# Optimization experiments

Hardware: AMD Instinct MI355X
Metric: run time of the kernel (lower is better)

Reference implementation:

```python
import jax, jax.numpy as jnp
import numpy as np

EMBED_DIM = 256
NUM_HEADS = 4
HEAD_DIM = EMBED_DIM // NUM_HEADS
B, N0, N1 = 4, 2048, 2048


def setup_inputs() -> dict:
    key = jax.random.key(0)
    ks = jax.random.split(key, 16)
    d = EMBED_DIM
    s = 0.02
    return {
        "x0": jax.random.normal(ks[0], (B, N0, d), jnp.float32),
        "x1": jax.random.normal(ks[1], (B, N1, d), jnp.float32),
        "Wqk": jax.random.normal(ks[2], (d, d), jnp.float32) * s,
        "bqk": jnp.zeros((d,), jnp.float32),
        "Wv": jax.random.normal(ks[3], (d, d), jnp.float32) * s,
        "bv": jnp.zeros((d,), jnp.float32),
        "Wout": jax.random.normal(ks[4], (d, d), jnp.float32) * s,
        "bout": jnp.zeros((d,), jnp.float32),
        "W0": jax.random.normal(ks[5], (2 * d, 2 * d), jnp.float32) * s,
        "b0": jnp.zeros((2 * d,), jnp.float32),
        "ln_scale": jnp.ones((2 * d,), jnp.float32),
        "ln_bias": jnp.zeros((2 * d,), jnp.float32),
        "W3": jax.random.normal(ks[6], (2 * d, d), jnp.float32) * s,
        "b3": jnp.zeros((d,), jnp.float32),
    }


def _heads(t, b, n):
    # [b, n, d] -> [b, h, n, hd]
    return t.reshape(b, n, NUM_HEADS, HEAD_DIM).transpose(0, 2, 1, 3)


def _layernorm(y, scale, bias, eps=1e-5):
    mu = jnp.mean(y, axis=-1, keepdims=True)
    var = jnp.mean(jnp.square(y - mu), axis=-1, keepdims=True)
    return (y - mu) * jax.lax.rsqrt(var + eps) * scale + bias


def reference(x0, x1, Wqk, bqk, Wv, bv, Wout, bout, W0, b0, ln_scale, ln_bias, W3, b3):
    b, n0, d = x0.shape
    _, n1, _ = x1.shape
    scale = 1.0 / jnp.sqrt(jnp.float32(HEAD_DIM))

    qk0 = _heads(x0 @ Wqk + bqk, b, n0)
    qk1 = _heads(x1 @ Wqk + bqk, b, n1)
    v0 = _heads(x0 @ Wv + bv, b, n0)
    v1 = _heads(x1 @ Wv + bv, b, n1)

    # shared logits: [b, h, n0, n1]
    logits01 = jnp.einsum('bhid,bhjd->bhij', qk0, qk1) * scale
    attn01 = jax.nn.softmax(logits01, axis=-1)
    m0 = jnp.einsum('bhij,bhjd->bhid', attn01, v1)
    attn10 = jax.nn.softmax(logits01.transpose(0, 1, 3, 2), axis=-1)
    m1 = jnp.einsum('bhji,bhjd->bhid', attn10.transpose(0, 1, 3, 2), v0)

    m0 = m0.transpose(0, 2, 1, 3).reshape(b, n0, d) @ Wout + bout
    m1 = m1.transpose(0, 2, 1, 3).reshape(b, n1, d) @ Wout + bout

    def ffn(x, m):
        y = jnp.concatenate([x, m], axis=-1) @ W0 + b0
        y = _layernorm(y, ln_scale, ln_bias)
        y = jax.nn.gelu(y, approximate=False)
        return x + y @ W3 + b3

    return ffn(x0, m0), ffn(x1, m1)
```

## Files before the change

### kernel.cpp

```cpp
#include <hip/hip_runtime.h>
#include <math.h>

#define BATCH 4
#define SEQ 2048
#define DMODEL 256
#define NH 4
#define HD 64
#define MROWS 8192
#define QKSCALE 0.4246608905f

typedef short bf16x8 __attribute__((ext_vector_type(8)));
typedef float f32x4 __attribute__((ext_vector_type(4)));
typedef unsigned short us;

#if __has_builtin(__builtin_amdgcn_exp2f)
#define EXP2(x) __builtin_amdgcn_exp2f(x)
#else
#define EXP2(x) exp2f(x)
#endif

__device__ __forceinline__ us f2bf(float x) {
  union { float f; unsigned int u; } v;
  v.f = x;
  unsigned int r = (v.u + 0x7FFF + ((v.u >> 16) & 1)) >> 16;
  return (us)r;
}
__device__ __forceinline__ float bf2f(us u) {
  union { unsigned int u; float f; } v;
  v.u = ((unsigned int)u) << 16;
  return v.f;
}
__device__ __forceinline__ unsigned int fbits(float x) {
  union { float f; unsigned int u; } v;
  v.f = x;
  return v.u;
}
__device__ __forceinline__ unsigned int pk2bf(float lo, float hi) {
  return __builtin_amdgcn_perm(fbits(hi), fbits(lo), 0x07060302u);
}
__device__ __forceinline__ void dma16(const void* g, void* l) {
  auto gp = (const __attribute__((address_space(1))) unsigned int*)(unsigned long long)(uintptr_t)g;
  auto lp = (__attribute__((address_space(3))) unsigned int*)(unsigned int)(uintptr_t)l;
  __builtin_amdgcn_global_load_lds(gp, lp, 16, 0, 0);
}

__global__ __launch_bounds__(256) void prep_k(
    const float* __restrict__ x0, const float* __restrict__ x1,
    const float* __restrict__ Wqk, const float* __restrict__ Wv,
    const float* __restrict__ W0, const float* __restrict__ W3,
    const float* __restrict__ Wout,
    const float* __restrict__ bqk, const float* __restrict__ bv,
    const float* __restrict__ b0, const float* __restrict__ bout,
    us* __restrict__ x0b, us* __restrict__ x1b,
    us* __restrict__ Wqvt, us* __restrict__ W1t, us* __restrict__ W3t,
    float* __restrict__ bias_qv, float* __restrict__ bias1) {
  const int bid = blockIdx.x, t = threadIdx.x;
  if (bid < 4096) {
    const int n4 = (MROWS * DMODEL) / 4;
    int i = bid * 256 + t;
    const float* src = (i < n4) ? x0 : x1;
    us* dst = (i < n4) ? x0b : x1b;
    int j = (i < n4) ? i : i - n4;
    float4 v = *(const float4*)&src[j * 4];
    ushort4 o = {f2bf(v.x), f2bf(v.y), f2bf(v.z), f2bf(v.w)};
    *(ushort4*)&dst[j * 4] = o;
  } else if (bid < 5634) {
    int gid = (bid - 4096) * 256 + t;
    if (gid < 65536) {
      int k = gid >> 8, j = gid & 255;
      Wqvt[j * 256 + k] = f2bf(Wqk[gid]);
    } else if (gid < 131072) {
      int i = gid - 65536;
      int k = i >> 8, j = i & 255;
      Wqvt[(256 + j) * 256 + k] = f2bf(Wv[i]);
    } else if (gid < 262144) {
      int i = gid - 131072;
      int k = i >> 9, j = i & 511;
      W1t[j * 512 + k] = f2bf(W0[i]);
    } else if (gid < 393216) {
      int i = gid - 262144;
      int k = i >> 8, j = i & 255;
      W3t[j * 512 + k] = f2bf(W3[i]);
    } else if (gid < 393728) {
      int j = gid - 393216;
      bias_qv[j] = (j < 256) ? bqk[j] : bv[j - 256];
    }
  } else {
    int i = bid - 5634;
    if (i < 256) {
      float a0 = 0.f, a1 = 0.f;
      for (int k0 = 0; k0 < 256; k0 += 8) {
        float wk[8], r0[8], r1[8];
#pragma unroll
        for (int u = 0; u < 8; ++u) {
          wk[u] = Wout[i * 256 + k0 + u];
          const float* row = &W0[(size_t)(256 + k0 + u) * 512];
          r0[u] = row[t];
          r1[u] = row[t + 256];
        }
#pragma unroll
        for (int u = 0; u < 8; ++u) { a0 += wk[u] * r0[u]; a1 += wk[u] * r1[u]; }
      }
      W1t[t * 512 + 256 + i] = f2bf(a0);
      W1t[(t + 256) * 512 + 256 + i] = f2bf(a1);
    } else {
      float a0 = b0[t], a1 = b0[t + 256];
      for (int k = 0; k < 256; ++k) {
        float bk = bout[k];
        const float* row = &W0[(size_t)(256 + k) * 512];
        a0 += bk * row[t];
        a1 += bk * row[t + 256];
      }
      bias1[t] = a0;
      bias1[t + 256] = a1;
    }
  }
}

template <int MODE>
__global__ __launch_bounds__(256) void gemm6(
    const us* __restrict__ A0, const us* __restrict__ A1,
    const us* __restrict__ Am0, const us* __restrict__ Am1,
    const us* __restrict__ Wt, const float* __restrict__ bias,
    const float* __restrict__ r0_, const float* __restrict__ r1_,
    void* __restrict__ C0_, void* __restrict__ C1_,
    void* __restrict__ V0_, void* __restrict__ V1_, int K) {
  constexpr int CT = (MODE == 2) ? 64 : 128;
  constexpr int BG = (CT / 16) * 2;
  constexpr int BUFS = 8192 + BG * 512;
  __shared__ us lds[2 * BUFS];

  const int t = threadIdx.x, w = t >> 6, lane = t & 63;
  const int qd = lane >> 4, l15 = lane & 15;

  const int flat = blockIdx.x + 64 * (blockIdx.y + 4 * blockIdx.z);
  const int xcd = flat & 7, slot = flat >> 3;
  const int xz = (xcd << 4) + (slot >> 2);
  const int bx = xz & 63, z = xz >> 6, coltile = slot & 3;
  const int row0 = bx * 128, col0 = coltile * CT;

  const us* Ax = z ? A1 : A0;
  const us* Am = z ? Am1 : Am0;
  const int qr = (MODE == 2) ? w : (w >> 1);
  const int qc = (MODE == 2) ? 0 : (w & 1);
  constexpr int MI = (MODE == 2) ? 2 : 4;

  f32x4 acc[MI][4];
#pragma unroll
  for (int i = 0; i < MI; ++i)
#pragma unroll
    for (int j = 0; j < 4; ++j) acc[i][j] = (f32x4){0.f, 0.f, 0.f, 0.f};

  const int NK = K >> 6;
#pragma unroll
  for (int pp = 0; pp < (16 + BG) / 4; ++pp) {
    int g = pp * 4 + w;
    const us* src;
    if (g < 16) {
      int tm = g >> 1, s = g & 1;
      int kk = s * 32 + qd * 8;
      src = &Ax[(size_t)(row0 + tm * 16 + l15) * ((MODE == 1) ? 256 : K) + kk];
    } else {
      int gb = g - 16, tn = gb >> 1, s = gb & 1;
      src = &Wt[(size_t)(col0 + tn * 16 + l15) * K + s * 32 + qd * 8];
    }
    dma16(src, &lds[g * 512]);
  }
  __syncthreads();

  int bsel = 0;
  for (int it = 0; it < NK; ++it) {
    if (it + 1 < NK) {
      int k0 = (it + 1) << 6;
#pragma unroll
      for (int pp = 0; pp < (16 + BG) / 4; ++pp) {
        int g = pp * 4 + w;
        const us* src;
        if (g < 16) {
          int tm = g >> 1, s = g & 1;
          const us* Ap = Ax;
          int kk = k0 + s * 32 + qd * 8, lda = K;
          if (MODE == 1) {
            Ap = (k0 < 256) ? Ax : Am;
            kk &= 255;
            lda = 256;
          }
          src = &Ap[(size_t)(row0 + tm * 16 + l15) * lda + kk];
        } else {
          int gb = g - 16, tn = gb >> 1, s = gb & 1;
          src = &Wt[(size_t)(col0 + tn * 16 + l15) * K + k0 + s * 32 + qd * 8];
        }
        dma16(src, &lds[(bsel ^ 1) * BUFS + g * 512]);
      }
    }
    const us* L = &lds[bsel * BUFS];
#pragma unroll
    for (int s = 0; s < 2; ++s) {
      bf16x8 af[MI], bfr[4];
#pragma unroll
      for (int i = 0; i < MI; ++i)
        af[i] = *(const bf16x8*)&L[(((qr * MI + i) * 2 + s) * 64 + lane) * 8];
#pragma unroll
      for (int j = 0; j < 4; ++j)
        bfr[j] = *(const bf16x8*)&L[8192 + (((qc * 4 + j) * 2 + s) * 64 + lane) * 8];
#pragma unroll
      for (int i = 0; i < MI; ++i)
#pragma unroll
        for (int j = 0; j < 4; ++j)
          acc[i][j] = __builtin_amdgcn_mfma_f32_16x16x32_bf16(af[i], bfr[j], acc[i][j], 0, 0, 0);
    }
    __syncthreads();
    bsel ^= 1;
  }

  if (MODE == 0 && coltile >= 2) {
    int base = qc * 8320;
#pragma unroll
    for (int j = 0; j < 4; ++j) {
      int col = col0 + qc * 64 + j * 16 + l15;
      float bb = bias[col];
#pragma unroll
      for (int i = 0; i < 4; ++i)
#pragma unroll
        for (int r = 0; r < 4; ++r)
          lds[base + (j * 16 + l15) * 130 + (qr * 64 + i * 16 + qd * 4 + r)] =
              f2bf(acc[i][j][r] + bb);
    }
    __syncthreads();
    us* Vt = (us*)(z ? V1_ : V0_);
    int b_ = row0 >> 11, seq0 = row0 & 2047;
    for (int c = t; c < 2048; c += 256) {
      int hh = c >> 10, cc = c & 1023;
      int dloc = cc >> 4, scc = cc & 15;
      int h = (coltile - 2) * 2 + hh;
      uint4 d = *(const uint4*)&lds[hh * 8320 + dloc * 130 + scc * 8];
      *(uint4*)&Vt[((size_t)(b_ * NH + h) * HD + dloc) * SEQ + seq0 + scc * 8] = d;
    }
    return;
  }

  if (MODE == 0 || MODE == 1) {
#pragma unroll
    for (int j = 0; j < 4; ++j) {
      int cl = qc * 64 + j * 16 + l15;
      float bb = bias[col0 + cl];
#pragma unroll
      for (int i = 0; i < 4; ++i)
#pragma unroll
        for (int r = 0; r < 4; ++r) {
          float v = acc[i][j][r] + bb;
          if (MODE == 0) v *= QKSCALE;
          lds[(qr * 64 + i * 16 + qd * 4 + r) * 132 + cl] = f2bf(v);
        }
    }
    __syncthreads();
    us* C = (us*)(z ? C1_ : C0_);
    const int ldc = (MODE == 0) ? 256 : 512;
    for (int c = t; c < 2048; c += 256) {
      int rl = c >> 4, c8 = (c & 15) * 8;
      uint4 d = *(const uint4*)&lds[rl * 132 + c8];
      *(uint4*)&C[(size_t)(row0 + rl) * ldc + col0 + c8] = d;
    }
    return;
  }

#pragma unroll
  for (int j = 0; j < 4; ++j) {
    int col = col0 + j * 16 + l15;
    float bb = bias[col];
#pragma unroll
    for (int i = 0; i < MI; ++i)
#pragma unroll
      for (int r = 0; r < 4; ++r) {
        size_t grow = row0 + qr * (MI * 16) + i * 16 + qd * 4 + r;
        const float* R = z ? r1_ : r0_;
        ((float*)(z ? C1_ : C0_))[grow * 256 + col] =
            R[grow * 256 + col] + acc[i][j][r] + bb;
      }
  }
}

__global__ __launch_bounds__(256) void flash_v7(
    const us* __restrict__ qk0, const us* __restrict__ qk1,
    const us* __restrict__ vt0, const us* __restrict__ vt1,
    float* __restrict__ Opart, float* __restrict__ lpart) {
  __shared__ us lds[16384];
  const int t = threadIdx.x, w = t >> 6, lane = t & 63;
  const int qd = lane >> 4, l15 = lane & 15;

  const int flat = blockIdx.x + 32 * (blockIdx.y + 4 * blockIdx.z);
  const int xcd = flat & 7, slot = flat >> 3;
  const int combo = (xcd << 2) + (slot >> 5);
  const int qs = slot & 31;
  const int qt = qs & 15, half = qs >> 4;
  const int dir = combo >> 4, bh = combo & 15, b = bh >> 2, h = bh & 3;

  const us* Qb = dir ? qk1 : qk0;
  const us* Kb = dir ? qk0 : qk1;
  const us* Vt = dir ? vt0 : vt1;
  float* Op = Opart + (size_t)(dir * 2 + half) * (MROWS * DMODEL);
  float* lp = lpart + ((size_t)(dir * 2 + half) * NH + h) * MROWS;
  const size_t qrow0 = (size_t)b * SEQ + (size_t)qt * 128;
  const int hoff = h * HD;
  const us* vtb = Vt + (size_t)(b * NH + h) * HD * SEQ;
  const int kt0 = half * 16;

  const us* sp[4];
  int sstr[4];
#pragma unroll
  for (int pp = 0; pp < 4; ++pp) {
    int g = pp * 4 + w;
    if (g < 8) {
      int tk = g >> 1, s = g & 1;
      int kvl = (tk >> 1) * 32 + (l15 >> 2) * 8 + (tk & 1) * 4 + (l15 & 3);
      sp[pp] = &Kb[(size_t)(b * SEQ + kt0 * 64 + kvl) * DMODEL + hoff + s * 32 + qd * 8];
      sstr[pp] = 64 * DMODEL;
    } else {
      int td = (g - 8) >> 1, s = g & 1;
      sp[pp] = &vtb[(size_t)(td * 16 + l15) * SEQ + kt0 * 64 + s * 32 + qd * 8];
      sstr[pp] = 64;
    }
  }

  bf16x8 qf[2][2];
#pragma unroll
  for (int qh = 0; qh < 2; ++qh)
#pragma unroll
    for (int s = 0; s < 2; ++s)
      qf[qh][s] = *(const bf16x8*)&Qb[(qrow0 + w * 32 + qh * 16 + l15) * DMODEL + hoff + s * 32 + qd * 8];

  f32x4 Oacc[2][4];
#pragma unroll
  for (int qh = 0; qh < 2; ++qh)
#pragma unroll
    for (int td = 0; td < 4; ++td) Oacc[qh][td] = (f32x4){0.f, 0.f, 0.f, 0.f};
  float l_lane[2] = {0.f, 0.f};

#pragma unroll
  for (int pp = 0; pp < 4; ++pp) {
    dma16(sp[pp], &lds[(pp * 4 + w) * 512]);
    sp[pp] += sstr[pp];
  }
  __syncthreads();

  int bsel = 0;
  for (int it = 0; it < 16; ++it) {
    if (it < 15) {
#pragma unroll
      for (int pp = 0; pp < 4; ++pp) {
        dma16(sp[pp], &lds[(bsel ^ 1) * 8192 + (pp * 4 + w) * 512]);
        sp[pp] += sstr[pp];
      }
    }
    const us* L = &lds[bsel * 8192];

    bf16x8 kf[4][2], vf[4][2];
#pragma unroll
    for (int tk = 0; tk < 4; ++tk)
#pragma unroll
      for (int s = 0; s < 2; ++s) {
        kf[tk][s] = *(const bf16x8*)&L[((tk * 2 + s) * 64 + lane) * 8];
        vf[tk][s] = *(const bf16x8*)&L[((8 + tk * 2 + s) * 64 + lane) * 8];
      }

#pragma unroll
    for (int qh = 0; qh < 2; ++qh) {
      f32x4 S[4];
#pragma unroll
      for (int tk = 0; tk < 4; ++tk) {
        f32x4 a = {0.f, 0.f, 0.f, 0.f};
        a = __builtin_amdgcn_mfma_f32_16x16x32_bf16(kf[tk][0], qf[qh][0], a, 0, 0, 0);
        a = __builtin_amdgcn_mfma_f32_16x16x32_bf16(kf[tk][1], qf[qh][1], a, 0, 0, 0);
        S[tk] = a;
      }
      float p[4][4];
      float rs = 0.f;
#pragma unroll
      for (int tk = 0; tk < 4; ++tk)
#pragma unroll
        for (int r = 0; r < 4; ++r) {
          float pv = EXP2(S[tk][r]);
          p[tk][r] = pv;
          rs += pv;
        }
      l_lane[qh] += rs;
      union { bf16x8 v; unsigned int u[4]; } pk0, pk1;
      pk0.u[0] = pk2bf(p[0][0], p[0][1]);
      pk0.u[1] = pk2bf(p[0][2], p[0][3]);
      pk0.u[2] = pk2bf(p[1][0], p[1][1]);
      pk0.u[3] = pk2bf(p[1][2], p[1][3]);
      pk1.u[0] = pk2bf(p[2][0], p[2][1]);
      pk1.u[1] = pk2bf(p[2][2], p[2][3]);
      pk1.u[2] = pk2bf(p[3][0], p[3][1]);
      pk1.u[3] = pk2bf(p[3][2], p[3][3]);
#pragma unroll
      for (int td = 0; td < 4; ++td) {
        Oacc[qh][td] = __builtin_amdgcn_mfma_f32_16x16x32_bf16(pk0.v, vf[td][0], Oacc[qh][td], 0, 0, 0);
        Oacc[qh][td] = __builtin_amdgcn_mfma_f32_16x16x32_bf16(pk1.v, vf[td][1], Oacc[qh][td], 0, 0, 0);
      }
    }
    __syncthreads();
    bsel ^= 1;
  }

#pragma unroll
  for (int qh = 0; qh < 2; ++qh) {
    float l = l_lane[qh];
    l += __shfl_xor(l, 16);
    l += __shfl_xor(l, 32);
    if (qd == 0) lp[qrow0 + w * 32 + qh * 16 + l15] = l;
#pragma unroll
    for (int r = 0; r < 4; ++r) {
      size_t row = qrow0 + w * 32 + qh * 16 + qd * 4 + r;
#pragma unroll
      for (int td = 0; td < 4; ++td)
        Op[row * DMODEL + hoff + td * 16 + l15] = Oacc[qh][td][r];
    }
  }
}

__global__ __launch_bounds__(256) void combine_k(
    const float* __restrict__ Opart, const float* __restrict__ lpart,
    us* __restrict__ m0b, us* __restrict__ m1b) {
  int gid = blockIdx.x * 256 + threadIdx.x;
  int dir = gid >= (MROWS * DMODEL / 4);
  int idx = gid - dir * (MROWS * DMODEL / 4);
  int row = idx >> 6;
  int c4 = (idx & 63) << 2;
  int h = c4 >> 6;
  const float* Oa = Opart + (size_t)(dir * 2 + 0) * (MROWS * DMODEL);
  const float* Ob = Opart + (size_t)(dir * 2 + 1) * (MROWS * DMODEL);
  float la = lpart[((size_t)(dir * 2 + 0) * NH + h) * MROWS + row];
  float lb = lpart[((size_t)(dir * 2 + 1) * NH + h) * MROWS + row];
  float inv = 1.0f / (la + lb);
  float4 a = *(const float4*)&Oa[(size_t)row * DMODEL + c4];
  float4 bv = *(const float4*)&Ob[(size_t)row * DMODEL + c4];
  us* m = dir ? m1b : m0b;
  ushort4 o = {f2bf((a.x + bv.x) * inv), f2bf((a.y + bv.y) * inv),
               f2bf((a.z + bv.z) * inv), f2bf((a.w + bv.w) * inv)};
  *(ushort4*)&m[(size_t)row * DMODEL + c4] = o;
}

__global__ __launch_bounds__(256) void ln_gelu3(
    us* __restrict__ Y0, us* __restrict__ Y1,
    const float* __restrict__ sc, const float* __restrict__ bi) {
  int w = threadIdx.x >> 6, lane = threadIdx.x & 63;
  int ridx = blockIdx.x * 4 + w;
  us* Y = (ridx >= MROWS) ? Y1 : Y0;
  int row = ridx & (MROWS - 1);
  us* p = Y + (size_t)row * 512 + lane * 8;
  uint4 u = *(const uint4*)p;
  unsigned int uu[4] = {u.x, u.y, u.z, u.w};
  float v[8];
#pragma unroll
  for (int i = 0; i < 4; ++i) {
    v[2 * i] = bf2f((us)(uu[i] & 0xFFFF));
    v[2 * i + 1] = bf2f((us)(uu[i] >> 16));
  }
  float s1 = 0.f, s2 = 0.f;
#pragma unroll
  for (int i = 0; i < 8; ++i) { s1 += v[i]; s2 += v[i] * v[i]; }
#pragma unroll
  for (int m = 1; m < 64; m <<= 1) {
    s1 += __shfl_xor(s1, m);
    s2 += __shfl_xor(s2, m);
  }
  float mu = s1 * (1.0f / 512.0f);
  float var = s2 * (1.0f / 512.0f) - mu * mu;
  float rstd = rsqrtf(var + 1e-5f);
  int c0 = lane * 8;
  float4 scA = *(const float4*)&sc[c0], scB = *(const float4*)&sc[c0 + 4];
  float4 biA = *(const float4*)&bi[c0], biB = *(const float4*)&bi[c0 + 4];
  float scv[8] = {scA.x, scA.y, scA.z, scA.w, scB.x, scB.y, scB.z, scB.w};
  float biv[8] = {biA.x, biA.y, biA.z, biA.w, biB.x, biB.y, biB.z, biB.w};
  unsigned int ou[4];
#pragma unroll
  for (int i = 0; i < 4; ++i) {
    float y0 = (v[2 * i] - mu) * rstd * scv[2 * i] + biv[2 * i];
    float y1 = (v[2 * i + 1] - mu) * rstd * scv[2 * i + 1] + biv[2 * i + 1];
    y0 = 0.5f * y0 * (1.0f + erff(y0 * 0.70710678118654752f));
    y1 = 0.5f * y1 * (1.0f + erff(y1 * 0.70710678118654752f));
    ou[i] = (unsigned int)f2bf(y0) | ((unsigned int)f2bf(y1) << 16);
  }
  uint4 o = {ou[0], ou[1], ou[2], ou[3]};
  *(uint4*)p = o;
}

extern "C" void kernel_launch(void* const* d_in, const int* in_sizes, int n_in,
                              void* d_out, int out_size, void* d_ws,
                              size_t ws_size, hipStream_t stream) {
  const float* x0   = (const float*)d_in[0];
  const float* x1   = (const float*)d_in[1];
  const float* Wqk  = (const float*)d_in[2];
  const float* bqk  = (const float*)d_in[3];
  const float* Wv   = (const float*)d_in[4];
  const float* bv   = (const float*)d_in[5];
  const float* Wout = (const float*)d_in[6];
  const float* bout = (const float*)d_in[7];
  const float* W0   = (const float*)d_in[8];
  const float* b0   = (const float*)d_in[9];
  const float* lns  = (const float*)d_in[10];
  const float* lnb  = (const float*)d_in[11];
  const float* W3   = (const float*)d_in[12];
  const float* b3   = (const float*)d_in[13];

  char* ws = (char*)d_ws;
  const size_t MB = 1024 * 1024;
  us* x0b  = (us*)(ws + 0 * MB);
  us* x1b  = (us*)(ws + 4 * MB);
  us* Wqvt = (us*)(ws + 8 * MB);
  us* W1t  = (us*)(ws + 8 * MB + 262144);
  us* W3t  = (us*)(ws + 8 * MB + 786432);
  float* bias_qv = (float*)(ws + 9 * MB);
  float* bias1   = (float*)(ws + 9 * MB + 4096);
  us* qk0b = (us*)(ws + 10 * MB);
  us* qk1b = (us*)(ws + 14 * MB);
  us* vt0  = (us*)(ws + 18 * MB);
  us* vt1  = (us*)(ws + 22 * MB);
  us* m0b  = (us*)(ws + 26 * MB);
  us* m1b  = (us*)(ws + 30 * MB);
  us* y0b  = (us*)(ws + 10 * MB);
  us* y1b  = (us*)(ws + 18 * MB);
  float* Opart = (float*)(ws + 34 * MB);
  float* lpart = (float*)(ws + 66 * MB);
  float* out0 = (float*)d_out;
  float* out1 = out0 + (size_t)MROWS * DMODEL;

  dim3 blk(256);

  prep_k<<<dim3(5891), blk, 0, stream>>>(x0, x1, Wqk, Wv, W0, W3, Wout,
                                         bqk, bv, b0, bout,
                                         x0b, x1b, Wqvt, W1t, W3t,
                                         bias_qv, bias1);

  gemm6<0><<<dim3(64, 4, 2), blk, 0, stream>>>(
      x0b, x1b, nullptr, nullptr, Wqvt, bias_qv, nullptr, nullptr,
      qk0b, qk1b, vt0, vt1, 256);

  flash_v7<<<dim3(32, 4, 8), blk, 0, stream>>>(qk0b, qk1b, vt0, vt1, Opart, lpart);
  combine_k<<<dim3(4096), blk, 0, stream>>>(Opart, lpart, m0b, m1b);

  gemm6<1><<<dim3(64, 4, 2), blk, 0, stream>>>(
      x0b, x1b, m0b, m1b, W1t, bias1, nullptr, nullptr,
      y0b, y1b, nullptr, nullptr, 512);

  ln_gelu3<<<dim3(4096), blk, 0, stream>>>(y0b, y1b, lns, lnb);

  gemm6<2><<<dim3(64, 4, 2), blk, 0, stream>>>(
      y0b, y1b, nullptr, nullptr, W3t, b3, x0, x1,
      out0, out1, nullptr, nullptr, 512);
}
```

Baseline: 234.8 us.

## Fuse split-KV combine into flash kernel and LayerNorm-GELU into FFN GEMMs

```diff
diff --git a/kernel.cpp b/kernel.cpp
--- a/kernel.cpp
+++ b/kernel.cpp
@@ -53,7 +53,8 @@
     const float* __restrict__ b0, const float* __restrict__ bout,
     us* __restrict__ x0b, us* __restrict__ x1b,
     us* __restrict__ Wqvt, us* __restrict__ W1t, us* __restrict__ W3t,
-    float* __restrict__ bias_qv, float* __restrict__ bias1) {
+    float* __restrict__ bias_qv, float* __restrict__ bias1,
+    float* __restrict__ zbase) {
   const int bid = blockIdx.x, t = threadIdx.x;
   if (bid < 4096) {
     const int n4 = (MROWS * DMODEL) / 4;
@@ -85,7 +86,7 @@
       int j = gid - 393216;
       bias_qv[j] = (j < 256) ? bqk[j] : bv[j - 256];
     }
-  } else {
+  } else if (bid < 5891) {
     int i = bid - 5634;
     if (i < 256) {
       float a0 = 0.f, a1 = 0.f;
@@ -114,6 +115,12 @@
       bias1[t] = a0;
       bias1[t + 256] = a1;
     }
+  } else {
+    int i = (bid - 5891) * 256 + t;
+    if (i * 4 < 33792) {
+      float4 zz = {0.f, 0.f, 0.f, 0.f};
+      *(float4*)&zbase[i * 4] = zz;
+    }
   }
 }
 
@@ -122,12 +129,10 @@
     const us* __restrict__ A0, const us* __restrict__ A1,
     const us* __restrict__ Am0, const us* __restrict__ Am1,
     const us* __restrict__ Wt, const float* __restrict__ bias,
-    const float* __restrict__ r0_, const float* __restrict__ r1_,
     void* __restrict__ C0_, void* __restrict__ C1_,
-    void* __restrict__ V0_, void* __restrict__ V1_, int K) {
-  constexpr int CT = (MODE == 2) ? 64 : 128;
-  constexpr int BG = (CT / 16) * 2;
-  constexpr int BUFS = 8192 + BG * 512;
+    void* __restrict__ V0_, void* __restrict__ V1_, int K,
+    float* __restrict__ lnsum, float* __restrict__ lnsq) {
+  constexpr int BUFS = 16384;
   __shared__ us lds[2 * BUFS];
 
   const int t = threadIdx.x, w = t >> 6, lane = t & 63;
@@ -137,29 +142,26 @@
   const int xcd = flat & 7, slot = flat >> 3;
   const int xz = (xcd << 4) + (slot >> 2);
   const int bx = xz & 63, z = xz >> 6, coltile = slot & 3;
-  const int row0 = bx * 128, col0 = coltile * CT;
+  const int row0 = bx * 128, col0 = coltile * 128;
 
   const us* Ax = z ? A1 : A0;
   const us* Am = z ? Am1 : Am0;
-  const int qr = (MODE == 2) ? w : (w >> 1);
-  const int qc = (MODE == 2) ? 0 : (w & 1);
-  constexpr int MI = (MODE == 2) ? 2 : 4;
-
-  f32x4 acc[MI][4];
-#pragma unroll
-  for (int i = 0; i < MI; ++i)
+  const int qr = w >> 1, qc = w & 1;
+
+  f32x4 acc[4][4];
+#pragma unroll
+  for (int i = 0; i < 4; ++i)
 #pragma unroll
     for (int j = 0; j < 4; ++j) acc[i][j] = (f32x4){0.f, 0.f, 0.f, 0.f};
 
   const int NK = K >> 6;
 #pragma unroll
-  for (int pp = 0; pp < (16 + BG) / 4; ++pp) {
+  for (int pp = 0; pp < 8; ++pp) {
     int g = pp * 4 + w;
     const us* src;
     if (g < 16) {
       int tm = g >> 1, s = g & 1;
-      int kk = s * 32 + qd * 8;
-      src = &Ax[(size_t)(row0 + tm * 16 + l15) * ((MODE == 1) ? 256 : K) + kk];
+      src = &Ax[(size_t)(row0 + tm * 16 + l15) * ((MODE == 1) ? 256 : K) + s * 32 + qd * 8];
     } else {
       int gb = g - 16, tn = gb >> 1, s = gb & 1;
       src = &Wt[(size_t)(col0 + tn * 16 + l15) * K + s * 32 + qd * 8];
@@ -173,7 +175,7 @@
     if (it + 1 < NK) {
       int k0 = (it + 1) << 6;
 #pragma unroll
-      for (int pp = 0; pp < (16 + BG) / 4; ++pp) {
+      for (int pp = 0; pp < 8; ++pp) {
         int g = pp * 4 + w;
         const us* src;
         if (g < 16) {
@@ -196,15 +198,14 @@
     const us* L = &lds[bsel * BUFS];
 #pragma unroll
     for (int s = 0; s < 2; ++s) {
-      bf16x8 af[MI], bfr[4];
-#pragma unroll
-      for (int i = 0; i < MI; ++i)
-        af[i] = *(const bf16x8*)&L[(((qr * MI + i) * 2 + s) * 64 + lane) * 8];
-#pragma unroll
-      for (int j = 0; j < 4; ++j)
-        bfr[j] = *(const bf16x8*)&L[8192 + (((qc * 4 + j) * 2 + s) * 64 + lane) * 8];
-#pragma unroll
-      for (int i = 0; i < MI; ++i)
+      bf16x8 af[4], bfr[4];
+#pragma unroll
+      for (int i = 0; i < 4; ++i) {
+        af[i] = *(const bf16x8*)&L[(((qr * 4 + i) * 2 + s) * 64 + lane) * 8];
+        bfr[i] = *(const bf16x8*)&L[8192 + (((qc * 4 + i) * 2 + s) * 64 + lane) * 8];
+      }
+#pragma unroll
+      for (int i = 0; i < 4; ++i)
 #pragma unroll
         for (int j = 0; j < 4; ++j)
           acc[i][j] = __builtin_amdgcn_mfma_f32_16x16x32_bf16(af[i], bfr[j], acc[i][j], 0, 0, 0);
@@ -239,52 +240,59 @@
     return;
   }
 
-  if (MODE == 0 || MODE == 1) {
-#pragma unroll
-    for (int j = 0; j < 4; ++j) {
-      int cl = qc * 64 + j * 16 + l15;
-      float bb = bias[col0 + cl];
-#pragma unroll
-      for (int i = 0; i < 4; ++i)
-#pragma unroll
-        for (int r = 0; r < 4; ++r) {
-          float v = acc[i][j][r] + bb;
-          if (MODE == 0) v *= QKSCALE;
-          lds[(qr * 64 + i * 16 + qd * 4 + r) * 132 + cl] = f2bf(v);
-        }
-    }
-    __syncthreads();
-    us* C = (us*)(z ? C1_ : C0_);
-    const int ldc = (MODE == 0) ? 256 : 512;
-    for (int c = t; c < 2048; c += 256) {
-      int rl = c >> 4, c8 = (c & 15) * 8;
-      uint4 d = *(const uint4*)&lds[rl * 132 + c8];
-      *(uint4*)&C[(size_t)(row0 + rl) * ldc + col0 + c8] = d;
-    }
-    return;
-  }
-
 #pragma unroll
   for (int j = 0; j < 4; ++j) {
-    int col = col0 + j * 16 + l15;
-    float bb = bias[col];
-#pragma unroll
-    for (int i = 0; i < MI; ++i)
+    int cl = qc * 64 + j * 16 + l15;
+    float bb = bias[col0 + cl];
+#pragma unroll
+    for (int i = 0; i < 4; ++i)
 #pragma unroll
       for (int r = 0; r < 4; ++r) {
-        size_t grow = row0 + qr * (MI * 16) + i * 16 + qd * 4 + r;
-        const float* R = z ? r1_ : r0_;
-        ((float*)(z ? C1_ : C0_))[grow * 256 + col] =
-            R[grow * 256 + col] + acc[i][j][r] + bb;
-      }
-  }
-}
-
-__global__ __launch_bounds__(256) void flash_v7(
+        float v = acc[i][j][r] + bb;
+        if (MODE == 0) v *= QKSCALE;
+        lds[(qr * 64 + i * 16 + qd * 4 + r) * 132 + cl] = f2bf(v);
+      }
+  }
+  __syncthreads();
+  us* C = (us*)(z ? C1_ : C0_);
+  const int ldc = (MODE == 0) ? 256 : 512;
+  for (int c = t; c < 2048; c += 256) {
+    int rl = c >> 4, c8 = (c & 15) * 8;
+    uint4 d = *(const uint4*)&lds[rl * 132 + c8];
+    *(uint4*)&C[(size_t)(row0 + rl) * ldc + col0 + c8] = d;
+  }
+
+  if (MODE == 1) {
+    int rl = t >> 1, hf = t & 1;
+    float s1 = 0.f, s2 = 0.f;
+#pragma unroll
+    for (int c = 0; c < 64; c += 8) {
+      uint4 d = *(const uint4*)&lds[rl * 132 + hf * 64 + c];
+      unsigned int uu[4] = {d.x, d.y, d.z, d.w};
+#pragma unroll
+      for (int i = 0; i < 4; ++i) {
+        float a = bf2f((us)(uu[i] & 0xFFFF));
+        float b = bf2f((us)(uu[i] >> 16));
+        s1 += a + b;
+        s2 += a * a + b * b;
+      }
+    }
+    s1 += __shfl_xor(s1, 1);
+    s2 += __shfl_xor(s2, 1);
+    if (hf == 0) {
+      atomicAdd(&lnsum[z * MROWS + row0 + rl], s1);
+      atomicAdd(&lnsq[z * MROWS + row0 + rl], s2);
+    }
+  }
+}
+
+__global__ __launch_bounds__(256) void flash_v8(
     const us* __restrict__ qk0, const us* __restrict__ qk1,
     const us* __restrict__ vt0, const us* __restrict__ vt1,
-    float* __restrict__ Opart, float* __restrict__ lpart) {
+    float* __restrict__ Opart, float* __restrict__ lpart,
+    us* __restrict__ m0b, us* __restrict__ m1b, int* __restrict__ tickets) {
   __shared__ us lds[16384];
+  __shared__ int sOld;
   const int t = threadIdx.x, w = t >> 6, lane = t & 63;
   const int qd = lane >> 4, l15 = lane & 15;
 
@@ -403,11 +411,13 @@
     bsel ^= 1;
   }
 
+  float lred[2];
 #pragma unroll
   for (int qh = 0; qh < 2; ++qh) {
     float l = l_lane[qh];
     l += __shfl_xor(l, 16);
     l += __shfl_xor(l, 32);
+    lred[qh] = l;
     if (qd == 0) lp[qrow0 + w * 32 + qh * 16 + l15] = l;
 #pragma unroll
     for (int r = 0; r < 4; ++r) {
@@ -417,73 +427,137 @@
         Op[row * DMODEL + hoff + td * 16 + l15] = Oacc[qh][td][r];
     }
   }
-}
-
-__global__ __launch_bounds__(256) void combine_k(
-    const float* __restrict__ Opart, const float* __restrict__ lpart,
-    us* __restrict__ m0b, us* __restrict__ m1b) {
-  int gid = blockIdx.x * 256 + threadIdx.x;
-  int dir = gid >= (MROWS * DMODEL / 4);
-  int idx = gid - dir * (MROWS * DMODEL / 4);
-  int row = idx >> 6;
-  int c4 = (idx & 63) << 2;
-  int h = c4 >> 6;
-  const float* Oa = Opart + (size_t)(dir * 2 + 0) * (MROWS * DMODEL);
-  const float* Ob = Opart + (size_t)(dir * 2 + 1) * (MROWS * DMODEL);
-  float la = lpart[((size_t)(dir * 2 + 0) * NH + h) * MROWS + row];
-  float lb = lpart[((size_t)(dir * 2 + 1) * NH + h) * MROWS + row];
-  float inv = 1.0f / (la + lb);
-  float4 a = *(const float4*)&Oa[(size_t)row * DMODEL + c4];
-  float4 bv = *(const float4*)&Ob[(size_t)row * DMODEL + c4];
-  us* m = dir ? m1b : m0b;
-  ushort4 o = {f2bf((a.x + bv.x) * inv), f2bf((a.y + bv.y) * inv),
-               f2bf((a.z + bv.z) * inv), f2bf((a.w + bv.w) * inv)};
-  *(ushort4*)&m[(size_t)row * DMODEL + c4] = o;
-}
-
-__global__ __launch_bounds__(256) void ln_gelu3(
-    us* __restrict__ Y0, us* __restrict__ Y1,
+
+  __threadfence();
+  __syncthreads();
+  if (t == 0) sOld = atomicAdd(&tickets[((dir * BATCH + b) * NH + h) * 16 + qt], 1);
+  __syncthreads();
+  if (sOld == 1) {
+    __threadfence();
+    us* m = dir ? m1b : m0b;
+    const float* Opp = Opart + (size_t)(dir * 2 + (half ^ 1)) * (MROWS * DMODEL);
+    const float* lpp = lpart + ((size_t)(dir * 2 + (half ^ 1)) * NH + h) * MROWS;
+#pragma unroll
+    for (int qh = 0; qh < 2; ++qh) {
+      float inv = 1.0f / (lred[qh] + lpp[qrow0 + w * 32 + qh * 16 + l15]);
+#pragma unroll
+      for (int r = 0; r < 4; ++r) {
+        float lq = __shfl(inv, qd * 20 + r, 64);
+        size_t row = qrow0 + w * 32 + qh * 16 + qd * 4 + r;
+#pragma unroll
+        for (int td = 0; td < 4; ++td) {
+          float o = Oacc[qh][td][r] + Opp[row * DMODEL + hoff + td * 16 + l15];
+          m[row * DMODEL + hoff + td * 16 + l15] = f2bf(o * lq);
+        }
+      }
+    }
+  }
+}
+
+__global__ __launch_bounds__(256) void ffn2_k(
+    const us* __restrict__ y0b, const us* __restrict__ y1b,
+    const us* __restrict__ W3t, const float* __restrict__ b3,
+    const float* __restrict__ x0, const float* __restrict__ x1,
+    float* __restrict__ out0, float* __restrict__ out1,
+    const float* __restrict__ lnsum, const float* __restrict__ lnsq,
     const float* __restrict__ sc, const float* __restrict__ bi) {
-  int w = threadIdx.x >> 6, lane = threadIdx.x & 63;
-  int ridx = blockIdx.x * 4 + w;
-  us* Y = (ridx >= MROWS) ? Y1 : Y0;
-  int row = ridx & (MROWS - 1);
-  us* p = Y + (size_t)row * 512 + lane * 8;
-  uint4 u = *(const uint4*)p;
-  unsigned int uu[4] = {u.x, u.y, u.z, u.w};
-  float v[8];
-#pragma unroll
-  for (int i = 0; i < 4; ++i) {
-    v[2 * i] = bf2f((us)(uu[i] & 0xFFFF));
-    v[2 * i + 1] = bf2f((us)(uu[i] >> 16));
-  }
-  float s1 = 0.f, s2 = 0.f;
-#pragma unroll
-  for (int i = 0; i < 8; ++i) { s1 += v[i]; s2 += v[i] * v[i]; }
-#pragma unroll
-  for (int m = 1; m < 64; m <<= 1) {
-    s1 += __shfl_xor(s1, m);
-    s2 += __shfl_xor(s2, m);
-  }
-  float mu = s1 * (1.0f / 512.0f);
-  float var = s2 * (1.0f / 512.0f) - mu * mu;
-  float rstd = rsqrtf(var + 1e-5f);
-  int c0 = lane * 8;
-  float4 scA = *(const float4*)&sc[c0], scB = *(const float4*)&sc[c0 + 4];
-  float4 biA = *(const float4*)&bi[c0], biB = *(const float4*)&bi[c0 + 4];
-  float scv[8] = {scA.x, scA.y, scA.z, scA.w, scB.x, scB.y, scB.z, scB.w};
-  float biv[8] = {biA.x, biA.y, biA.z, biA.w, biB.x, biB.y, biB.z, biB.w};
-  unsigned int ou[4];
-#pragma unroll
-  for (int i = 0; i < 4; ++i) {
-    float y0 = (v[2 * i] - mu) * rstd * scv[2 * i] + biv[2 * i];
-    float y1 = (v[2 * i + 1] - mu) * rstd * scv[2 * i + 1] + biv[2 * i + 1];
-    y0 = 0.5f * y0 * (1.0f + erff(y0 * 0.70710678118654752f));
-    y1 = 0.5f * y1 * (1.0f + erff(y1 * 0.70710678118654752f));
-    ou[i] = (unsigned int)f2bf(y0) | ((unsigned int)f2bf(y1) << 16);
-  }
-  uint4 o = {ou[0], ou[1], ou[2], ou[3]};
-  *(uint4*)p = o;
+  constexpr int BUFS = 12288;
+  __shared__ us lds[2 * BUFS];
+  const int t = threadIdx.x, w = t >> 6, lane = t & 63;
+  const int qd = lane >> 4, l15 = lane & 15;
+
+  const int flat = blockIdx.x + 128 * (blockIdx.y + 2 * blockIdx.z);
+  const int xcd = flat & 7, slot = flat >> 3;
+  const int xz = xcd * 32 + (slot >> 1);
+  const int bx = xz & 127, z = xz >> 7, ct = slot & 1;
+  const int row0 = bx * 64, col0 = ct * 128;
+
+  const us* Y = z ? y1b : y0b;
+  const float* lsum = lnsum + z * MROWS;
+  const float* lsq = lnsq + z * MROWS;
+  const int qr = w >> 1, qc = w & 1;
+
+  f32x4 acc[2][4];
+#pragma unroll
+  for (int i = 0; i < 2; ++i)
+#pragma unroll
+    for (int j = 0; j < 4; ++j) acc[i][j] = (f32x4){0.f, 0.f, 0.f, 0.f};
+
+  auto stage = [&](int k0, us* buf) {
+#pragma unroll
+    for (int pp = 0; pp < 4; ++pp) {
+      int gb = pp * 4 + w;
+      int tn = gb >> 1, s = gb & 1;
+      dma16(&W3t[(size_t)(col0 + tn * 16 + l15) * 512 + k0 + s * 32 + qd * 8],
+            &buf[4096 + gb * 512]);
+    }
+#pragma unroll
+    for (int pp = 0; pp < 2; ++pp) {
+      int g = pp * 4 + w;
+      int tm = g >> 1, s = g & 1;
+      int row = row0 + tm * 16 + l15;
+      int kk = k0 + s * 32 + qd * 8;
+      uint4 d = *(const uint4*)&Y[(size_t)row * 512 + kk];
+      float mu = lsum[row] * (1.0f / 512.0f);
+      float vr = lsq[row] * (1.0f / 512.0f) - mu * mu;
+      float rstd = rsqrtf(vr + 1e-5f);
+      unsigned int uu[4] = {d.x, d.y, d.z, d.w};
+      unsigned int ou[4];
+#pragma unroll
+      for (int i = 0; i < 4; ++i) {
+        int k_ = kk + 2 * i;
+        float a = bf2f((us)(uu[i] & 0xFFFF));
+        float bq = bf2f((us)(uu[i] >> 16));
+        float g0 = (a - mu) * rstd * sc[k_] + bi[k_];
+        float g1 = (bq - mu) * rstd * sc[k_ + 1] + bi[k_ + 1];
+        g0 = 0.5f * g0 * (1.0f + erff(g0 * 0.70710678118654752f));
+        g1 = 0.5f * g1 * (1.0f + erff(g1 * 0.70710678118654752f));
+        ou[i] = pk2bf(g0, g1);
+      }
+      uint4 o = {ou[0], ou[1], ou[2], ou[3]};
+      *(uint4*)&buf[g * 512 + lane * 8] = o;
+    }
+  };
+
+  stage(0, lds);
+  __syncthreads();
+  int bsel = 0;
+  for (int it = 0; it < 8; ++it) {
+    if (it < 7) stage((it + 1) * 64, &lds[(bsel ^ 1) * BUFS]);
+    const us* L = &lds[bsel * BUFS];
+#pragma unroll
+    for (int s = 0; s < 2; ++s) {
+      bf16x8 af[2], bfr[4];
+#pragma unroll
+      for (int i = 0; i < 2; ++i)
+        af[i] = *(const bf16x8*)&L[(((qr * 2 + i) * 2 + s) * 64 + lane) * 8];
+#pragma unroll
+      for (int j = 0; j < 4; ++j)
+        bfr[j] = *(const bf16x8*)&L[4096 + (((qc * 4 + j) * 2 + s) * 64 + lane) * 8];
+#pragma unroll
+      for (int i = 0; i < 2; ++i)
+#pragma unroll
+        for (int j = 0; j < 4; ++j)
+          acc[i][j] = __builtin_amdgcn_mfma_f32_16x16x32_bf16(af[i], bfr[j], acc[i][j], 0, 0, 0);
+    }
+    __syncthreads();
+    bsel ^= 1;
+  }
+
+  const float* X = z ? x1 : x0;
+  float* O = z ? out1 : out0;
+#pragma unroll
+  for (int j = 0; j < 4; ++j) {
+    int col = col0 + qc * 64 + j * 16 + l15;
+    float bb = b3[col];
+#pragma unroll
+    for (int i = 0; i < 2; ++i)
+#pragma unroll
+      for (int r = 0; r < 4; ++r) {
+        size_t grow = row0 + qr * 32 + i * 16 + qd * 4 + r;
+        O[grow * 256 + col] = X[grow * 256 + col] + acc[i][j][r] + bb;
+      }
+  }
 }
 
 extern "C" void kernel_launch(void* const* d_in, const int* in_sizes, int n_in,
@@ -523,30 +597,31 @@
   us* y1b  = (us*)(ws + 18 * MB);
   float* Opart = (float*)(ws + 34 * MB);
   float* lpart = (float*)(ws + 66 * MB);
+  int* tickets = (int*)(ws + 66 * MB + 524288);
+  float* lnsum = (float*)(ws + 66 * MB + 528384);
+  float* lnsq  = lnsum + 2 * MROWS;
+  float* zbase = (float*)(ws + 66 * MB + 524288);
   float* out0 = (float*)d_out;
   float* out1 = out0 + (size_t)MROWS * DMODEL;
 
   dim3 blk(256);
 
-  prep_k<<<dim3(5891), blk, 0, stream>>>(x0, x1, Wqk, Wv, W0, W3, Wout,
+  prep_k<<<dim3(5924), blk, 0, stream>>>(x0, x1, Wqk, Wv, W0, W3, Wout,
                                          bqk, bv, b0, bout,
                                          x0b, x1b, Wqvt, W1t, W3t,
-                                         bias_qv, bias1);
+                                         bias_qv, bias1, zbase);
 
   gemm6<0><<<dim3(64, 4, 2), blk, 0, stream>>>(
-      x0b, x1b, nullptr, nullptr, Wqvt, bias_qv, nullptr, nullptr,
-      qk0b, qk1b, vt0, vt1, 256);
-
-  flash_v7<<<dim3(32, 4, 8), blk, 0, stream>>>(qk0b, qk1b, vt0, vt1, Opart, lpart);
-  combine_k<<<dim3(4096), blk, 0, stream>>>(Opart, lpart, m0b, m1b);
+      x0b, x1b, nullptr, nullptr, Wqvt, bias_qv,
+      qk0b, qk1b, vt0, vt1, 256, nullptr, nullptr);
+
+  flash_v8<<<dim3(32, 4, 8), blk, 0, stream>>>(qk0b, qk1b, vt0, vt1,
+                                               Opart, lpart, m0b, m1b, tickets);
 
   gemm6<1><<<dim3(64, 4, 2), blk, 0, stream>>>(
-      x0b, x1b, m0b, m1b, W1t, bias1, nullptr, nullptr,
-      y0b, y1b, nullptr, nullptr, 512);
-
-  ln_gelu3<<<dim3(4096), blk, 0, stream>>>(y0b, y1b, lns, lnb);
-
-  gemm6<2><<<dim3(64, 4, 2), blk, 0, stream>>>(
-      y0b, y1b, nullptr, nullptr, W3t, b3, x0, x1,
-      out0, out1, nullptr, nullptr, 512);
-}
+      x0b, x1b, m0b, m1b, W1t, bias1,
+      y0b, y1b, nullptr, nullptr, 512, lnsum, lnsq);
+
+  ffn2_k<<<dim3(128, 2, 2), blk, 0, stream>>>(
+      y0b, y1b, W3t, b3, x0, x1, out0, out1, lnsum, lnsq, lns, lnb);
+}
```

New measurement: 410.6 us. +74.9%, slower.
